# Kernel tuning notes

Hardware: AMD Instinct MI355X
Metric: run time of the kernel (lower is better)

## Reference

```python
import jax, jax.numpy as jnp
import numpy as np

B, C, H, W, HEADS = 4, 192, 128, 128, 8
C2 = 2 * C
DN = ('NCHW', 'OIHW', 'NCHW')


def conv1x1(x, w, b):
    o = jax.lax.conv_general_dilated(x, w, (1, 1), 'VALID', dimension_numbers=DN)
    return o + b[None, :, None, None]


def gconv3(x, w, b):
    # grouped 3x3 conv: groups = C, channels = 2C -> 2 in / 2 out channels per group
    o = jax.lax.conv_general_dilated(x, w, (1, 1), 'SAME', dimension_numbers=DN,
                                     feature_group_count=C)
    return o + b[None, :, None, None]


def l2norm(t):
    # torch F.normalize(dim=-1, eps=1e-12)
    n = jnp.linalg.norm(t, axis=-1, keepdims=True)
    return t / jnp.maximum(n, 1e-12)


def setup_inputs() -> dict:
    key = jax.random.key(0)
    ks = jax.random.split(key, 16)
    s = 0.02
    inp = {
        'x': jax.random.normal(ks[0], (B, C, H, W), jnp.float32),
        'y': jax.random.normal(ks[1], (B, C, H, W), jnp.float32),
        'kv_w': jax.random.normal(ks[2], (C2, C, 1, 1), jnp.float32) * s,
        'kv_b': jax.random.normal(ks[3], (C2,), jnp.float32) * s,
        'kv_dw_w': jax.random.normal(ks[4], (C2, 2, 3, 3), jnp.float32) * s,
        'kv_dw_b': jax.random.normal(ks[5], (C2,), jnp.float32) * s,
        'q_w': jax.random.normal(ks[6], (C2, C, 1, 1), jnp.float32) * s,
        'q_b': jax.random.normal(ks[7], (C2,), jnp.float32) * s,
        'q_dw_w': jax.random.normal(ks[8], (C2, 2, 3, 3), jnp.float32) * s,
        'q_dw_b': jax.random.normal(ks[9], (C2,), jnp.float32) * s,
        'ky_w': jax.random.normal(ks[10], (C2, C, 1, 1), jnp.float32) * s,
        'ky_b': jax.random.normal(ks[11], (C2,), jnp.float32) * s,
        'ky_dw_w': jax.random.normal(ks[12], (C2, 2, 3, 3), jnp.float32) * s,
        'ky_dw_b': jax.random.normal(ks[13], (C2,), jnp.float32) * s,
        'temperature': jnp.ones((HEADS, 1, 1), jnp.float32),
        'gamma1': jnp.full((1,), 0.1, jnp.float32),
        'gamma2': jnp.full((1,), 0.1, jnp.float32),
    }
    return inp


def reference(x, y, kv_w, kv_b, kv_dw_w, kv_dw_b, q_w, q_b, q_dw_w, q_dw_b,
              ky_w, ky_b, ky_dw_w, ky_dw_b, temperature, gamma1, gamma2):
    b, c, h, w = x.shape
    ch = c // HEADS  # channels per head

    x_mid = x + y
    q = gconv3(conv1x1(x_mid, kv_w, kv_b), kv_dw_w, kv_dw_b)
    q1, q2 = jnp.split(q, 2, axis=1)
    kvx = gconv3(conv1x1(x, q_w, q_b), q_dw_w, q_dw_b)
    kx, vx = jnp.split(kvx, 2, axis=1)
    kvy = gconv3(conv1x1(y, ky_w, ky_b), ky_dw_w, ky_dw_b)
    ky_, vy = jnp.split(kvy, 2, axis=1)

    def to_heads(t):  # (b, head*ch, h, w) -> (b, head, ch, h*w)
        return t.reshape(b, HEADS, ch, h * w)

    q1, q2, kx, ky_, vx, vy = map(to_heads, (q1, q2, kx, ky_, vx, vy))
    q1, q2, kx, ky_ = map(l2norm, (q1, q2, kx, ky_))

    attn = (jnp.einsum('bhcn,bhdn->bhcd', q1, ky_) +
            jnp.einsum('bhcn,bhdn->bhcd', q2, kx)) * temperature[None]
    attn = jax.nn.softmax(attn, axis=-1)  # (b, head, c, c), tiny c

    out1 = jnp.einsum('bhcd,bhdn->bhcn', attn, vx)
    out2 = jnp.einsum('bhcd,bhdn->bhcn', attn, vy)
    out = gamma1[0] * out1 + gamma2[0] * out2
    return out.reshape(b, c, h, w)
```

## Files before the change

kernel.cpp:

```cpp
#include <hip/hip_runtime.h>
#include <hip/hip_bf16.h>
#include <stdint.h>

#define NUM_B 4
#define NUM_C 192
#define NUM_C2 384
#define NUM_H 128
#define NUM_W 128
#define NUM_N 16384
#define NHEADS 8
#define CHD 24

#define NKC 128
#define PSTRIDE 1280
#define LROWF 132

typedef float f32x4_t __attribute__((ext_vector_type(4)));
typedef float f32x2_t __attribute__((ext_vector_type(2)));
typedef __bf16 bf16x8_t __attribute__((ext_vector_type(8)));
typedef unsigned short u16x8_t __attribute__((ext_vector_type(8)));
typedef unsigned short u16x4_t __attribute__((ext_vector_type(4)));

__device__ __forceinline__ float bf2f(unsigned short u){
  union { unsigned int i; float f; } v; v.i = ((unsigned int)u) << 16; return v.f;
}
__device__ __forceinline__ unsigned short f2bf(float f){
  union { float f; unsigned int i; } v; v.f = f;
  unsigned int x = v.i;
  x += 0x7fffu + ((x >> 16) & 1u);
  return (unsigned short)(x >> 16);
}
__device__ __forceinline__ unsigned short f2bf_n(float f){
  union { __bf16 h; unsigned short u; } cv; cv.h = (__bf16)f; return cv.u;
}

__global__ __launch_bounds__(256) void prepack_all(
    const float* __restrict__ x, const float* __restrict__ y,
    const float* __restrict__ W0, const float* __restrict__ W1,
    const float* __restrict__ W2,
    unsigned short* __restrict__ xb, unsigned short* __restrict__ yb,
    unsigned short* __restrict__ Wpk)
{
  const int t = threadIdx.x;
  if (blockIdx.y == 6){
    int flat = blockIdx.z * 128 + blockIdx.x;
    if (flat >= 108) return;
    int gtid = flat * 256 + t;
    int br = gtid / 9216;
    int tid = gtid % 9216;
    const float* W = (br == 0) ? W0 : (br == 1) ? W1 : W2;
    unsigned short* o_ = Wpk + (size_t)br * 73728;
    int c = tid & 3;
    int o = (tid >> 2) & 127;
    int s = (tid >> 9) % 6;
    int ot = tid / 3072;
    int sw = c ^ ((o >> 1) & 3);
    const float* src = W + (size_t)(ot * 128 + o) * NUM_C + s * 32 + sw * 8;
    f32x4_t f0 = *(const f32x4_t*)src;
    f32x4_t f1 = *(const f32x4_t*)(src + 4);
    u16x8_t pk;
    pk[0] = f2bf(f0[0]); pk[1] = f2bf(f0[1]); pk[2] = f2bf(f0[2]); pk[3] = f2bf(f0[3]);
    pk[4] = f2bf(f1[0]); pk[5] = f2bf(f1[1]); pk[6] = f2bf(f1[2]); pk[7] = f2bf(f1[3]);
    *(u16x8_t*)(o_ + (size_t)tid * 8) = pk;
    return;
  }
  __shared__ __align__(16) float LX[32 * LROWF];
  __shared__ __align__(16) float LY[32 * LROWF];
  const int nt = blockIdx.x, s = blockIdx.y, b = blockIdx.z;
  const float* px = x + (size_t)b * NUM_C * NUM_N + (size_t)s * 32 * NUM_N + nt * 128;
  const float* py = y + (size_t)b * NUM_C * NUM_N + (size_t)s * 32 * NUM_N + nt * 128;
  #pragma unroll
  for (int i = 0; i < 4; i++){
    int idx = t + 256 * i;
    int k = idx >> 5, n4 = idx & 31;
    f32x4_t vx4 = *(const f32x4_t*)(px + (size_t)k * NUM_N + n4 * 4);
    f32x4_t vy4 = *(const f32x4_t*)(py + (size_t)k * NUM_N + n4 * 4);
    int col = (n4 * 4) ^ ((k >> 3) << 3);
    *(f32x4_t*)(&LX[k * LROWF + col]) = vx4;
    *(f32x4_t*)(&LY[k * LROWF + col]) = vy4;
  }
  __syncthreads();
  size_t obase = ((size_t)(b * 128 + nt) * 6 + s) * 4096;
  #pragma unroll
  for (int i = 0; i < 2; i++){
    int u = t + 256 * i;
    int n = u >> 2, slot = u & 3;
    int c = slot ^ ((n >> 1) & 3);
    int colr = n ^ (c << 3);
    u16x8_t ox, oy;
    #pragma unroll
    for (int kk = 0; kk < 8; kk++){
      ox[kk] = f2bf_n(LX[(c * 8 + kk) * LROWF + colr]);
      oy[kk] = f2bf_n(LY[(c * 8 + kk) * LROWF + colr]);
    }
    *(u16x8_t*)(xb + obase + (size_t)u * 8) = ox;
    *(u16x8_t*)(yb + obase + (size_t)u * 8) = oy;
  }
}

__global__ __launch_bounds__(256, 4) void conv1x1_fused(
    const unsigned short* __restrict__ xb, const unsigned short* __restrict__ yb,
    const unsigned short* __restrict__ Wpk,
    const float* __restrict__ b0, const float* __restrict__ b1,
    const float* __restrict__ b2, unsigned short* __restrict__ z3)
{
  __shared__ __align__(16) unsigned short As[2][4096];
  __shared__ __align__(16) unsigned short Bs[2][4096];
  const int d = blockIdx.x;
  const int xcd = d & 7;
  const int rest = d >> 3;
  const int j = rest % 9;
  const int m_ = (rest / 9) * 8 + xcd;
  const int br = j / 3;
  const int ot = j % 3;
  const int nt = m_ & 127;
  const int b  = m_ >> 7;
  const int t = threadIdx.x;
  const int lane = t & 63;
  const int wv = t >> 6;
  const int wr = wv >> 1, wc = wv & 1;
  const int n0 = nt * 128;

  const unsigned short* Bp0 = (br == 2) ? yb : xb;
  const unsigned short* Bp1 = yb;
  const int add2 = (br == 0);
  const unsigned short* Wb = Wpk + (size_t)br * 73728;
  const float* bias = (br == 0) ? b0 : (br == 1) ? b1 : b2;
  unsigned short* zout = z3 + (size_t)br * NUM_B * NUM_C2 * NUM_N;

  f32x4_t acc[4][4];
  const f32x4_t zz = {0.f, 0.f, 0.f, 0.f};
  #pragma unroll
  for (int m = 0; m < 4; m++)
    #pragma unroll
    for (int nf = 0; nf < 4; nf++) acc[m][nf] = zz;

  u16x8_t areg[2], breg[2], breg2[2];

  auto loadA = [&](int ks){
    const u16x8_t* gp = (const u16x8_t*)(Wb + (size_t)(ot * 6 + ks) * 4096);
    areg[0] = gp[t];
    areg[1] = gp[t + 256];
  };
  auto loadB = [&](int ks){
    size_t off = ((size_t)(b * 128 + nt) * 6 + ks) * 4096;
    const u16x8_t* gp = (const u16x8_t*)(Bp0 + off);
    breg[0] = gp[t];
    breg[1] = gp[t + 256];
    if (add2){
      const u16x8_t* gp2 = (const u16x8_t*)(Bp1 + off);
      breg2[0] = gp2[t];
      breg2[1] = gp2[t + 256];
    }
  };
  auto writeA = [&](int buf){
    *(u16x8_t*)(&As[buf][(size_t)t * 8]) = areg[0];
    *(u16x8_t*)(&As[buf][(size_t)(t + 256) * 8]) = areg[1];
  };
  auto writeB = [&](int buf){
    if (!add2){
      *(u16x8_t*)(&Bs[buf][(size_t)t * 8]) = breg[0];
      *(u16x8_t*)(&Bs[buf][(size_t)(t + 256) * 8]) = breg[1];
    } else {
      #pragma unroll
      for (int i = 0; i < 2; i++){
        u16x8_t r;
        #pragma unroll
        for (int jj = 0; jj < 8; jj++)
          r[jj] = f2bf_n(bf2f(breg[i][jj]) + bf2f(breg2[i][jj]));
        *(u16x8_t*)(&Bs[buf][(size_t)(t + 256 * i) * 8]) = r;
      }
    }
  };

  auto compute = [&](int buf){
    const int rsel = lane & 15;
    const int g = lane >> 4;
    bf16x8_t af[4], bfr[4];
    #pragma unroll
    for (int m = 0; m < 4; m++){
      int r = wr * 64 + m * 16 + rsel;
      int sw = g ^ ((r >> 1) & 3);
      af[m] = *(const bf16x8_t*)(&As[buf][r * 32 + sw * 8]);
    }
    #pragma unroll
    for (int nf = 0; nf < 4; nf++){
      int r = wc * 64 + nf * 16 + rsel;
      int sw = g ^ ((r >> 1) & 3);
      bfr[nf] = *(const bf16x8_t*)(&Bs[buf][r * 32 + sw * 8]);
    }
    #pragma unroll
    for (int m = 0; m < 4; m++)
      #pragma unroll
      for (int nf = 0; nf < 4; nf++)
        acc[m][nf] = __builtin_amdgcn_mfma_f32_16x16x32_bf16(af[m], bfr[nf], acc[m][nf], 0, 0, 0);
  };

  loadA(0); loadB(0);
  writeA(0); writeB(0);
  __syncthreads();
  int buf = 0;
  #pragma unroll 1
  for (int ks = 0; ks < 6; ks++){
    if (ks < 5){
      loadA(ks + 1);
      loadB(ks + 1);
    }
    compute(buf);
    if (ks < 5){
      writeA(buf ^ 1);
      writeB(buf ^ 1);
      __syncthreads();
    }
    buf ^= 1;
  }

  const int colb = lane & 15;
  const int ob_l = lane >> 4;
  #pragma unroll
  for (int m = 0; m < 4; m++){
    int o_blk = ot * 32 + wr * 16 + m * 4 + ob_l;
    #pragma unroll
    for (int nf = 0; nf < 4; nf++){
      int col = n0 + wc * 64 + nf * 16 + colb;
      u16x4_t pk;
      #pragma unroll
      for (int r = 0; r < 4; r++)
        pk[r] = f2bf_n(acc[m][nf][r] + bias[o_blk * 4 + r]);
      *(u16x4_t*)(zout + (((size_t)b * 96 + o_blk) * NUM_N + col) * 4) = pk;
    }
  }
}

__global__ __launch_bounds__(256) void gconv4_dw(
    const unsigned short* __restrict__ zp,
    const float* __restrict__ dww, const float* __restrict__ dwb,
    unsigned short* __restrict__ outq)
{
  const int t = threadIdx.x;
  const int wo = t & 15;
  const int hh = t >> 4;
  const int h = blockIdx.x * 16 + hh;
  const int g2 = blockIdx.y;
  const int b = blockIdx.z;

  float v[4][3][8];
  const unsigned short* src = zp + (size_t)(b * 96 + g2) * NUM_N * 4;
  #pragma unroll
  for (int dy = 0; dy < 3; dy++){
    int row = h + dy - 1;
    if (row >= 0 && row < NUM_H){
      const unsigned short* base = src + (size_t)(row * NUM_W + wo * 8) * 4;
      u16x8_t ch[4];
      #pragma unroll
      for (int q = 0; q < 4; q++) ch[q] = *(const u16x8_t*)(base + q * 8);
      #pragma unroll
      for (int jw = 0; jw < 8; jw++)
        #pragma unroll
        for (int c = 0; c < 4; c++){
          int idx = jw * 4 + c;
          v[c][dy][jw] = bf2f(ch[idx >> 3][idx & 7]);
        }
    } else {
      #pragma unroll
      for (int c = 0; c < 4; c++)
        #pragma unroll
        for (int jw = 0; jw < 8; jw++) v[c][dy][jw] = 0.f;
    }
  }
  float lft[4][3], rgt[4][3];
  #pragma unroll
  for (int c = 0; c < 4; c++)
    #pragma unroll
    for (int dy = 0; dy < 3; dy++){
      float l = __shfl_up(v[c][dy][7], 1u, 64);
      float r = __shfl_down(v[c][dy][0], 1u, 64);
      lft[c][dy] = (wo == 0)  ? 0.f : l;
      rgt[c][dy] = (wo == 15) ? 0.f : r;
    }
  #pragma unroll
  for (int c = 0; c < 4; c++){
    const int oc = g2 * 4 + c;
    const int ci0 = c & 2;
    float wgt[2][9];
    #pragma unroll
    for (int icg = 0; icg < 2; icg++)
      #pragma unroll
      for (int k9 = 0; k9 < 9; k9++)
        wgt[icg][k9] = dww[(size_t)oc * 18 + icg * 9 + k9];
    float bia = dwb[oc];
    u16x8_t st;
    #pragma unroll
    for (int w8 = 0; w8 < 8; w8++){
      float s = bia;
      #pragma unroll
      for (int icg = 0; icg < 2; icg++){
        const int ci = ci0 + icg;
        #pragma unroll
        for (int ky = 0; ky < 3; ky++)
          #pragma unroll
          for (int kx = 0; kx < 3; kx++){
            int wx = w8 + kx - 1;
            float xv = (wx < 0) ? lft[ci][ky] : ((wx > 7) ? rgt[ci][ky] : v[ci][ky][wx]);
            s += wgt[icg][ky * 3 + kx] * xv;
          }
      }
      st[w8] = f2bf(s);
    }
    *(u16x8_t*)(outq + ((size_t)b * NUM_C2 + oc) * NUM_N + h * NUM_W + wo * 8) = st;
  }
}

__global__ __launch_bounds__(64) void dots_kernel(
    const unsigned short* __restrict__ qkv0, const unsigned short* __restrict__ qkv1,
    const unsigned short* __restrict__ qkv2, float* __restrict__ dpart)
{
  const int lane = threadIdx.x;
  const int kc = blockIdx.x;
  const int h = blockIdx.y;
  const int b = blockIdx.z;
  const unsigned short* q1 = qkv0 + ((size_t)b * NUM_C2 + h * CHD) * NUM_N;
  const unsigned short* q2 = qkv0 + ((size_t)b * NUM_C2 + NUM_C + h * CHD) * NUM_N;
  const unsigned short* kx = qkv1 + ((size_t)b * NUM_C2 + h * CHD) * NUM_N;
  const unsigned short* ky = qkv2 + ((size_t)b * NUM_C2 + h * CHD) * NUM_N;

  const f32x4_t zz = {0.f, 0.f, 0.f, 0.f};
  f32x4_t d1[2][2], d2[2][2], nrm[4][2];
  #pragma unroll
  for (int i = 0; i < 2; i++)
    #pragma unroll
    for (int j = 0; j < 2; j++){ d1[i][j] = zz; d2[i][j] = zz; }
  #pragma unroll
  for (int tn = 0; tn < 4; tn++){ nrm[tn][0] = zz; nrm[tn][1] = zz; }

  const int row = lane & 15;
  const int kl = (lane >> 4) * 8;
  const int r0 = row;
  const int r1 = (16 + row < CHD) ? (16 + row) : (CHD - 1);
  #pragma unroll
  for (int ks = 0; ks < 4; ks++){
    const size_t k0 = (size_t)kc * 128 + ks * 32 + kl;
    const size_t off0 = (size_t)r0 * NUM_N + k0;
    const size_t off1 = (size_t)r1 * NUM_N + k0;
    bf16x8_t fq1[2], fq2[2], fkx[2], fky[2];
    fq1[0] = *(const bf16x8_t*)(q1 + off0);  fq1[1] = *(const bf16x8_t*)(q1 + off1);
    fq2[0] = *(const bf16x8_t*)(q2 + off0);  fq2[1] = *(const bf16x8_t*)(q2 + off1);
    fkx[0] = *(const bf16x8_t*)(kx + off0);  fkx[1] = *(const bf16x8_t*)(kx + off1);
    fky[0] = *(const bf16x8_t*)(ky + off0);  fky[1] = *(const bf16x8_t*)(ky + off1);
    #pragma unroll
    for (int i = 0; i < 2; i++)
      #pragma unroll
      for (int j = 0; j < 2; j++){
        d1[i][j] = __builtin_amdgcn_mfma_f32_16x16x32_bf16(fq1[i], fky[j], d1[i][j], 0, 0, 0);
        d2[i][j] = __builtin_amdgcn_mfma_f32_16x16x32_bf16(fq2[i], fkx[j], d2[i][j], 0, 0, 0);
      }
    #pragma unroll
    for (int rg = 0; rg < 2; rg++){
      nrm[0][rg] = __builtin_amdgcn_mfma_f32_16x16x32_bf16(fq1[rg], fq1[rg], nrm[0][rg], 0, 0, 0);
      nrm[1][rg] = __builtin_amdgcn_mfma_f32_16x16x32_bf16(fq2[rg], fq2[rg], nrm[1][rg], 0, 0, 0);
      nrm[2][rg] = __builtin_amdgcn_mfma_f32_16x16x32_bf16(fkx[rg], fkx[rg], nrm[2][rg], 0, 0, 0);
      nrm[3][rg] = __builtin_amdgcn_mfma_f32_16x16x32_bf16(fky[rg], fky[rg], nrm[3][rg], 0, 0, 0);
    }
  }

  float* P = dpart + ((size_t)kc * (NUM_B * NHEADS) + (b * NHEADS + h)) * PSTRIDE;
  const int colb = lane & 15;
  const int rb = (lane >> 4) * 4;
  #pragma unroll
  for (int i = 0; i < 2; i++)
    #pragma unroll
    for (int j = 0; j < 2; j++){
      int cc = j * 16 + colb;
      if (cc < CHD){
        #pragma unroll
        for (int r = 0; r < 4; r++){
          int rr = i * 16 + rb + r;
          if (rr < CHD){
            P[rr * CHD + cc] = d1[i][j][r];
            P[576 + rr * CHD + cc] = d2[i][j][r];
          }
        }
      }
    }
  #pragma unroll
  for (int tn = 0; tn < 4; tn++)
    #pragma unroll
    for (int rg = 0; rg < 2; rg++){
      int cc = rg * 16 + colb;
      #pragma unroll
      for (int r = 0; r < 4; r++){
        int rr = rg * 16 + rb + r;
        if (rr == cc && rr < CHD) P[1152 + tn * CHD + rr] = nrm[tn][rg][r];
      }
    }
}

__global__ __launch_bounds__(256) void reduce_dots(
    const float* __restrict__ dpart,
    float* __restrict__ dots1, float* __restrict__ dots2, float* __restrict__ norms)
{
  const int slot = blockIdx.x * 256 + threadIdx.x;
  const int bh = blockIdx.y;
  if (slot >= 1248) return;
  float s = 0.f;
  #pragma unroll 4
  for (int kc = 0; kc < NKC; kc++)
    s += dpart[((size_t)kc * (NUM_B * NHEADS) + bh) * PSTRIDE + slot];
  if (slot < 576)        dots1[(size_t)bh * 576 + slot] = s;
  else if (slot < 1152)  dots2[(size_t)bh * 576 + (slot - 576)] = s;
  else                   norms[(size_t)bh * 96 + (slot - 1152)] = s;
}

__global__ __launch_bounds__(64) void softmax_kernel(
    const float* __restrict__ dots1, const float* __restrict__ dots2,
    const float* __restrict__ norms, const float* __restrict__ temp,
    float* __restrict__ attn)
{
  const int c = threadIdx.x;
  const int bh = blockIdx.x;
  if (c >= CHD) return;
  const int h = bh & 7;
  const float* D1 = dots1 + (size_t)bh * CHD * CHD;
  const float* D2 = dots2 + (size_t)bh * CHD * CHD;
  const float* NB = norms + (size_t)bh * 4 * CHD;
  float n1 = fmaxf(sqrtf(NB[0 * CHD + c]), 1e-12f);
  float n2 = fmaxf(sqrtf(NB[1 * CHD + c]), 1e-12f);
  float T = temp[h];
  float l[CHD];
  float m = -1e30f;
  #pragma unroll
  for (int d = 0; d < CHD; d++){
    float nx = fmaxf(sqrtf(NB[2 * CHD + d]), 1e-12f);
    float ny = fmaxf(sqrtf(NB[3 * CHD + d]), 1e-12f);
    float e = (D1[c * CHD + d] / (n1 * ny) + D2[c * CHD + d] / (n2 * nx)) * T;
    l[d] = e; m = fmaxf(m, e);
  }
  float s = 0.f;
  #pragma unroll
  for (int d = 0; d < CHD; d++){ float p = expf(l[d] - m); l[d] = p; s += p; }
  float inv = 1.f / s;
  float* A = attn + (size_t)bh * CHD * CHD + c * CHD;
  #pragma unroll
  for (int d = 0; d < CHD; d++) A[d] = l[d] * inv;
}

__global__ __launch_bounds__(256) void out_kernel(
    const unsigned short* __restrict__ qkv1, const unsigned short* __restrict__ qkv2,
    const float* __restrict__ attn,
    const float* __restrict__ g1, const float* __restrict__ g2,
    float* __restrict__ out)
{
  __shared__ float A[CHD * CHD];
  const int t = threadIdx.x;
  const int nc = blockIdx.x, hq = blockIdx.y, b = blockIdx.z;
  const float* Ag = attn + (size_t)(b * NHEADS + hq) * CHD * CHD;
  for (int i = t; i < CHD * CHD; i += 256) A[i] = Ag[i];
  __syncthreads();
  const int n = nc * 512 + t * 2;
  const unsigned short* vx = qkv1 + ((size_t)b * NUM_C2 + NUM_C + hq * CHD) * NUM_N + n;
  const unsigned short* vy = qkv2 + ((size_t)b * NUM_C2 + NUM_C + hq * CHD) * NUM_N + n;
  float vxa[CHD], vxb[CHD], vya[CHD], vyb[CHD];
  #pragma unroll
  for (int d = 0; d < CHD; d++){
    unsigned int rx = *(const unsigned int*)(vx + (size_t)d * NUM_N);
    unsigned int ry = *(const unsigned int*)(vy + (size_t)d * NUM_N);
    vxa[d] = bf2f((unsigned short)(rx & 0xffffu));
    vxb[d] = bf2f((unsigned short)(rx >> 16));
    vya[d] = bf2f((unsigned short)(ry & 0xffffu));
    vyb[d] = bf2f((unsigned short)(ry >> 16));
  }
  const float G1 = g1[0], G2 = g2[0];
  float* ob = out + ((size_t)b * NUM_C + hq * CHD) * NUM_N + n;
  #pragma unroll
  for (int cq = 0; cq < CHD; cq++){
    float ax = 0.f, bx = 0.f, ay = 0.f, by = 0.f;
    #pragma unroll
    for (int d = 0; d < CHD; d++){
      float a = A[cq * CHD + d];
      ax += a * vxa[d]; bx += a * vxb[d];
      ay += a * vya[d]; by += a * vyb[d];
    }
    f32x2_t st = {G1 * ax + G2 * ay, G1 * bx + G2 * by};
    *(f32x2_t*)(ob + (size_t)cq * NUM_N) = st;
  }
}

extern "C" void kernel_launch(void* const* d_in, const int* in_sizes, int n_in,
                              void* d_out, int out_size, void* d_ws, size_t ws_size,
                              hipStream_t stream)
{
  const float* x = (const float*)d_in[0];
  const float* y = (const float*)d_in[1];
  const float* conv_b[3] = {(const float*)d_in[3], (const float*)d_in[7], (const float*)d_in[11]};
  const float* dw_w[3]   = {(const float*)d_in[4], (const float*)d_in[8], (const float*)d_in[12]};
  const float* dw_b[3]   = {(const float*)d_in[5], (const float*)d_in[9], (const float*)d_in[13]};
  const float* conv_w[3] = {(const float*)d_in[2], (const float*)d_in[6], (const float*)d_in[10]};
  const float* temp = (const float*)d_in[14];
  const float* g1 = (const float*)d_in[15];
  const float* g2 = (const float*)d_in[16];
  float* out = (float*)d_out;

  char* ws = (char*)d_ws;
  const size_t ZB = (size_t)NUM_B * NUM_C2 * NUM_N * 2;
  unsigned short* xb   = (unsigned short*)ws;
  unsigned short* yb   = (unsigned short*)(ws + 25165824);
  unsigned short* z3   = (unsigned short*)(ws + 50331648);
  unsigned short* qkv0 = (unsigned short*)ws;
  unsigned short* qkv1 = (unsigned short*)(ws + 50331648);
  unsigned short* qkv2 = (unsigned short*)(ws + 100663296);
  float* dpart         = (float*)(ws + 150994944);
  float* dots1 = (float*)(ws + 201326592);
  float* dots2 = dots1 + NUM_B * NHEADS * CHD * CHD;
  float* norms = dots2 + NUM_B * NHEADS * CHD * CHD;
  float* attn  = norms + NUM_B * NHEADS * 4 * CHD;
  unsigned short* Wpk = (unsigned short*)(attn + NUM_B * NHEADS * CHD * CHD);

  prepack_all<<<dim3(128, 7, NUM_B), 256, 0, stream>>>(
      x, y, conv_w[0], conv_w[1], conv_w[2], xb, yb, Wpk);

  conv1x1_fused<<<4608, 256, 0, stream>>>(xb, yb, Wpk,
                                          conv_b[0], conv_b[1], conv_b[2], z3);

  dim3 gd(NUM_H / 16, 96, NUM_B), bd(256);
  unsigned short* zb0 = z3;
  unsigned short* zb1 = z3 + ZB / 2;
  unsigned short* zb2 = z3 + ZB;
  gconv4_dw<<<gd, bd, 0, stream>>>(zb0, dw_w[0], dw_b[0], qkv0);
  gconv4_dw<<<gd, bd, 0, stream>>>(zb1, dw_w[1], dw_b[1], qkv1);
  gconv4_dw<<<gd, bd, 0, stream>>>(zb2, dw_w[2], dw_b[2], qkv2);

  dots_kernel<<<dim3(NKC, NHEADS, NUM_B), 64, 0, stream>>>(qkv0, qkv1, qkv2, dpart);
  reduce_dots<<<dim3(5, NUM_B * NHEADS), 256, 0, stream>>>(dpart, dots1, dots2, norms);
  softmax_kernel<<<dim3(NUM_B * NHEADS), 64, 0, stream>>>(dots1, dots2, norms, temp, attn);
  out_kernel<<<dim3(32, NHEADS, NUM_B), 256, 0, stream>>>(qkv1, qkv2, attn, g1, g2, out);
}
```

Baseline: 234.7 us.

## Deepen conv1x1 GEMM prefetch to two stages and fuse softmax into out kernel

The 1x1-conv GEMM now prefetches global tiles two k-steps ahead using double-buffered registers, and the main loop is fully unrolled, so more load latency can hide behind the MFMA work. The second operand for the summed x+y branch is still loaded one step ahead. Separately, the softmax kernel is removed and its work is redone redundantly inside each out_kernel block, writing the attention matrix straight to shared memory. This saves one launch and the attn buffer round trip, but costs extra registers in the GEMM and repeated softmax work across the 32 blocks per head.

```diff
diff --git a/kernel.cpp b/kernel.cpp
--- a/kernel.cpp
+++ b/kernel.cpp
@@ -135,39 +135,40 @@
     #pragma unroll
     for (int nf = 0; nf < 4; nf++) acc[m][nf] = zz;
 
-  u16x8_t areg[2], breg[2], breg2[2];
-
-  auto loadA = [&](int ks){
+  u16x8_t areg[2][2], breg[2][2], breg2[2];
+
+  auto loadA_s = [&](int ks, int s){
     const u16x8_t* gp = (const u16x8_t*)(Wb + (size_t)(ot * 6 + ks) * 4096);
-    areg[0] = gp[t];
-    areg[1] = gp[t + 256];
+    areg[s][0] = gp[t];
+    areg[s][1] = gp[t + 256];
   };
-  auto loadB = [&](int ks){
-    size_t off = ((size_t)(b * 128 + nt) * 6 + ks) * 4096;
-    const u16x8_t* gp = (const u16x8_t*)(Bp0 + off);
-    breg[0] = gp[t];
-    breg[1] = gp[t + 256];
+  auto loadB_s = [&](int ks, int s){
+    const u16x8_t* gp = (const u16x8_t*)(Bp0 + ((size_t)(b * 128 + nt) * 6 + ks) * 4096);
+    breg[s][0] = gp[t];
+    breg[s][1] = gp[t + 256];
+  };
+  auto loadB2 = [&](int ks){
     if (add2){
-      const u16x8_t* gp2 = (const u16x8_t*)(Bp1 + off);
+      const u16x8_t* gp2 = (const u16x8_t*)(Bp1 + ((size_t)(b * 128 + nt) * 6 + ks) * 4096);
       breg2[0] = gp2[t];
       breg2[1] = gp2[t + 256];
     }
   };
-  auto writeA = [&](int buf){
-    *(u16x8_t*)(&As[buf][(size_t)t * 8]) = areg[0];
-    *(u16x8_t*)(&As[buf][(size_t)(t + 256) * 8]) = areg[1];
+  auto writeA_s = [&](int s, int buf){
+    *(u16x8_t*)(&As[buf][(size_t)t * 8]) = areg[s][0];
+    *(u16x8_t*)(&As[buf][(size_t)(t + 256) * 8]) = areg[s][1];
   };
-  auto writeB = [&](int buf){
+  auto writeB_s = [&](int s, int buf){
     if (!add2){
-      *(u16x8_t*)(&Bs[buf][(size_t)t * 8]) = breg[0];
-      *(u16x8_t*)(&Bs[buf][(size_t)(t + 256) * 8]) = breg[1];
+      *(u16x8_t*)(&Bs[buf][(size_t)t * 8]) = breg[s][0];
+      *(u16x8_t*)(&Bs[buf][(size_t)(t + 256) * 8]) = breg[s][1];
     } else {
       #pragma unroll
       for (int i = 0; i < 2; i++){
         u16x8_t r;
         #pragma unroll
         for (int jj = 0; jj < 8; jj++)
-          r[jj] = f2bf_n(bf2f(breg[i][jj]) + bf2f(breg2[i][jj]));
+          r[jj] = f2bf_n(bf2f(breg[s][i][jj]) + bf2f(breg2[i][jj]));
         *(u16x8_t*)(&Bs[buf][(size_t)(t + 256 * i) * 8]) = r;
       }
     }
@@ -196,23 +197,24 @@
         acc[m][nf] = __builtin_amdgcn_mfma_f32_16x16x32_bf16(af[m], bfr[nf], acc[m][nf], 0, 0, 0);
   };
 
-  loadA(0); loadB(0);
-  writeA(0); writeB(0);
+  loadA_s(0, 0); loadB_s(0, 0); loadB2(0);
+  writeA_s(0, 0); writeB_s(0, 0);
+  loadA_s(1, 0); loadB_s(1, 0);
   __syncthreads();
-  int buf = 0;
-  #pragma unroll 1
+
+  #pragma unroll
   for (int ks = 0; ks < 6; ks++){
-    if (ks < 5){
-      loadA(ks + 1);
-      loadB(ks + 1);
-    }
-    compute(buf);
-    if (ks < 5){
-      writeA(buf ^ 1);
-      writeB(buf ^ 1);
+    if (ks + 1 <= 5) loadB2(ks + 1);
+    if (ks + 2 <= 5){
+      loadA_s(ks + 2, (ks + 1) & 1);
+      loadB_s(ks + 2, (ks + 1) & 1);
+    }
+    compute(ks & 1);
+    if (ks + 1 <= 5){
+      writeA_s(ks & 1, (ks + 1) & 1);
+      writeB_s(ks & 1, (ks + 1) & 1);
       __syncthreads();
     }
-    buf ^= 1;
   }
 
   const int colb = lane & 15;
@@ -411,50 +413,41 @@
   else                   norms[(size_t)bh * 96 + (slot - 1152)] = s;
 }
 
-__global__ __launch_bounds__(64) void softmax_kernel(
+__global__ __launch_bounds__(256) void out_kernel(
+    const unsigned short* __restrict__ qkv1, const unsigned short* __restrict__ qkv2,
     const float* __restrict__ dots1, const float* __restrict__ dots2,
     const float* __restrict__ norms, const float* __restrict__ temp,
-    float* __restrict__ attn)
-{
-  const int c = threadIdx.x;
-  const int bh = blockIdx.x;
-  if (c >= CHD) return;
-  const int h = bh & 7;
-  const float* D1 = dots1 + (size_t)bh * CHD * CHD;
-  const float* D2 = dots2 + (size_t)bh * CHD * CHD;
-  const float* NB = norms + (size_t)bh * 4 * CHD;
-  float n1 = fmaxf(sqrtf(NB[0 * CHD + c]), 1e-12f);
-  float n2 = fmaxf(sqrtf(NB[1 * CHD + c]), 1e-12f);
-  float T = temp[h];
-  float l[CHD];
-  float m = -1e30f;
-  #pragma unroll
-  for (int d = 0; d < CHD; d++){
-    float nx = fmaxf(sqrtf(NB[2 * CHD + d]), 1e-12f);
-    float ny = fmaxf(sqrtf(NB[3 * CHD + d]), 1e-12f);
-    float e = (D1[c * CHD + d] / (n1 * ny) + D2[c * CHD + d] / (n2 * nx)) * T;
-    l[d] = e; m = fmaxf(m, e);
-  }
-  float s = 0.f;
-  #pragma unroll
-  for (int d = 0; d < CHD; d++){ float p = expf(l[d] - m); l[d] = p; s += p; }
-  float inv = 1.f / s;
-  float* A = attn + (size_t)bh * CHD * CHD + c * CHD;
-  #pragma unroll
-  for (int d = 0; d < CHD; d++) A[d] = l[d] * inv;
-}
-
-__global__ __launch_bounds__(256) void out_kernel(
-    const unsigned short* __restrict__ qkv1, const unsigned short* __restrict__ qkv2,
-    const float* __restrict__ attn,
     const float* __restrict__ g1, const float* __restrict__ g2,
     float* __restrict__ out)
 {
   __shared__ float A[CHD * CHD];
   const int t = threadIdx.x;
   const int nc = blockIdx.x, hq = blockIdx.y, b = blockIdx.z;
-  const float* Ag = attn + (size_t)(b * NHEADS + hq) * CHD * CHD;
-  for (int i = t; i < CHD * CHD; i += 256) A[i] = Ag[i];
+  const int bh = b * NHEADS + hq;
+  if (t < CHD){
+    const int c = t;
+    const float* D1 = dots1 + (size_t)bh * CHD * CHD;
+    const float* D2 = dots2 + (size_t)bh * CHD * CHD;
+    const float* NB = norms + (size_t)bh * 4 * CHD;
+    float n1 = fmaxf(sqrtf(NB[0 * CHD + c]), 1e-12f);
+    float n2 = fmaxf(sqrtf(NB[1 * CHD + c]), 1e-12f);
+    float T = temp[hq];
+    float l[CHD];
+    float m = -1e30f;
+    #pragma unroll
+    for (int dd = 0; dd < CHD; dd++){
+      float nx = fmaxf(sqrtf(NB[2 * CHD + dd]), 1e-12f);
+      float ny = fmaxf(sqrtf(NB[3 * CHD + dd]), 1e-12f);
+      float e = (D1[c * CHD + dd] / (n1 * ny) + D2[c * CHD + dd] / (n2 * nx)) * T;
+      l[dd] = e; m = fmaxf(m, e);
+    }
+    float s = 0.f;
+    #pragma unroll
+    for (int dd = 0; dd < CHD; dd++){ float p = expf(l[dd] - m); l[dd] = p; s += p; }
+    float inv = 1.f / s;
+    #pragma unroll
+    for (int dd = 0; dd < CHD; dd++) A[c * CHD + dd] = l[dd] * inv;
+  }
   __syncthreads();
   const int n = nc * 512 + t * 2;
   const unsigned short* vx = qkv1 + ((size_t)b * NUM_C2 + NUM_C + hq * CHD) * NUM_N + n;
@@ -512,8 +505,7 @@
   float* dots1 = (float*)(ws + 201326592);
   float* dots2 = dots1 + NUM_B * NHEADS * CHD * CHD;
   float* norms = dots2 + NUM_B * NHEADS * CHD * CHD;
-  float* attn  = norms + NUM_B * NHEADS * 4 * CHD;
-  unsigned short* Wpk = (unsigned short*)(attn + NUM_B * NHEADS * CHD * CHD);
+  unsigned short* Wpk = (unsigned short*)(norms + NUM_B * NHEADS * 4 * CHD);
 
   prepack_all<<<dim3(128, 7, NUM_B), 256, 0, stream>>>(
       x, y, conv_w[0], conv_w[1], conv_w[2], xb, yb, Wpk);
@@ -531,6 +523,6 @@
 
   dots_kernel<<<dim3(NKC, NHEADS, NUM_B), 64, 0, stream>>>(qkv0, qkv1, qkv2, dpart);
   reduce_dots<<<dim3(5, NUM_B * NHEADS), 256, 0, stream>>>(dpart, dots1, dots2, norms);
-  softmax_kernel<<<dim3(NUM_B * NHEADS), 64, 0, stream>>>(dots1, dots2, norms, temp, attn);
-  out_kernel<<<dim3(32, NHEADS, NUM_B), 256, 0, stream>>>(qkv1, qkv2, attn, g1, g2, out);
-}
+  out_kernel<<<dim3(32, NHEADS, NUM_B), 256, 0, stream>>>(
+      qkv1, qkv2, dots1, dots2, norms, temp, g1, g2, out);
+}
```

After: 261.9 us. 11.6% more time.
